# Performance work log

Measured on AMD Instinct MI355X. Metric: run time of the kernel, lower is better.

Reference implementation:

```python
import jax, jax.numpy as jnp
import numpy as np

EPS = 1e-12

def _l2norm(v, axis):
    n = jnp.sqrt(jnp.sum(v * v, axis=axis, keepdims=True))
    return v / jnp.maximum(n, EPS)

def setup_inputs() -> dict:
    key = jax.random.key(0)
    k1, k2, k3, k4 = jax.random.split(key, 4)
    N, T, D, K = 8, 2048, 512, 64
    x = jax.random.normal(k1, (N, T, D), dtype=jnp.float32)
    W = jax.random.normal(k2, (K, D), dtype=jnp.float32) * (1.0 / np.sqrt(D))  # Conv1d(k=1) weight squeezed
    b = jax.random.normal(k3, (K,), dtype=jnp.float32) * 0.01
    centroids = jax.random.uniform(k4, (K, D), dtype=jnp.float32)
    return {"x": x, "W": W, "b": b, "centroids": centroids}

def reference(x, W, b, centroids):
    N, T, D = x.shape
    K = centroids.shape[0]
    # L2-normalize descriptors along feature dim
    xn = _l2norm(x, axis=2)                                  # [N,T,D]
    # Conv1d with kernel_size=1 == per-timestep linear: [N,K,T] logits over clusters
    logits = jnp.einsum('ntd,kd->nkt', xn, W) + b[None, :, None]
    a = jax.nn.softmax(logits, axis=1)                       # soft assignment over K
    # Algebraically equal to sum_t a[n,k,t] * (xn[n,t,:] - c[k,:])
    vlad = jnp.einsum('nkt,ntd->nkd', a, xn) \
         - jnp.sum(a, axis=2)[:, :, None] * centroids[None]  # [N,K,D]
    vlad = _l2norm(vlad, axis=2)                             # intra-normalize per cluster
    vlad = vlad.reshape(N, K * D)
    return _l2norm(vlad, axis=1)                             # global L2 normalize
```

## Files before the change

kernel.cpp:

```cpp
#include <hip/hip_runtime.h>
#include <math.h>

#define EPS 1e-12f
#define NN 8
#define TT 2048
#define DD 512
#define KK 64

typedef short short8 __attribute__((ext_vector_type(8)));
typedef float floatx4 __attribute__((ext_vector_type(4)));

__device__ __forceinline__ unsigned short f2bf(float f) {
    unsigned int u = __float_as_uint(f);
    u += 0x7FFFu + ((u >> 16) & 1u);
    return (unsigned short)(u >> 16);
}
__device__ __forceinline__ unsigned int pack2(float a, float b) {
    return (unsigned int)f2bf(a) | ((unsigned int)f2bf(b) << 16);
}
__device__ __forceinline__ float bf2f_lo(unsigned int u) {
    return __uint_as_float(u << 16);
}
__device__ __forceinline__ float bf2f_hi(unsigned int u) {
    return __uint_as_float(u & 0xFFFF0000u);
}


__global__ __launch_bounds__(1024) void kA(const float* __restrict__ x,
                                           const float* __restrict__ W,
                                           const float* __restrict__ bias,
                                           unsigned short* __restrict__ xb,
                                           unsigned short* __restrict__ aTs,
                                           float* __restrict__ asumP) {
    __shared__ unsigned short sW[32768];
    __shared__ unsigned short sX[32768];
    __shared__ float sSt[64];
    __shared__ float sM[4 * 64];
    __shared__ float sS[4 * 64];
    __shared__ float sRed[256];

    const int tid = threadIdx.x;
    const int w = tid >> 6, lane = tid & 63;
    const int l = lane & 15, q = lane >> 4;
    const int row0 = blockIdx.x * 64;
    const int n = row0 >> 11;
    const int tl0 = row0 & (TT - 1);

    float ssqr[4] = {0.f, 0.f, 0.f, 0.f};
#pragma unroll
    for (int i = 0; i < 8; ++i) {
        const int rl = w * 4 + (i >> 1);
        const int d0 = (i & 1) * 256 + lane * 4;
        float4 u = *(const float4*)(x + (size_t)(row0 + rl) * DD + d0);
        ssqr[i >> 1] += u.x * u.x + u.y * u.y + u.z * u.z + u.w * u.w;
        uint2 pk;
        pk.x = pack2(u.x, u.y);
        pk.y = pack2(u.z, u.w);
        *(uint2*)(xb + (size_t)(row0 + rl) * DD + d0) = pk;
        const int s0 = d0 >> 5, q0 = (d0 >> 3) & 3, half = (d0 >> 2) & 1;
        const int g0 = rl >> 4, lr = rl & 15;
        const int slot = ((g0 * 16 + s0) * 4 + q0) * 16 + (lr ^ ((s0 * 4 + q0) & 15));
        *(uint2*)(sX + slot * 8 + half * 4) = pk;
    }

#pragma unroll
    for (int j = 0; j < 4; ++j) {
        const int slot = tid * 4 + j;
        const int lw = slot & 15, qw = (slot >> 4) & 3, hw = (slot >> 6) & 3, sw = slot >> 8;
        const float* src = W + (size_t)(hw * 16 + lw) * DD + sw * 32 + qw * 8;
        float4 u0 = *(const float4*)(src);
        float4 u1 = *(const float4*)(src + 4);
        uint4 pk;
        pk.x = pack2(u0.x, u0.y); pk.y = pack2(u0.z, u0.w);
        pk.z = pack2(u1.x, u1.y); pk.w = pack2(u1.z, u1.w);
        const int sl2 = slot ^ ((slot >> 4) & 7);
        *(uint4*)(sW + sl2 * 8) = pk;
    }

#pragma unroll
    for (int rr = 0; rr < 4; ++rr) {
        float ss = ssqr[rr];
#pragma unroll
        for (int m = 1; m <= 32; m <<= 1) ss += __shfl_xor(ss, m, 64);
        if (lane == 0) sSt[w * 4 + rr] = 1.0f / fmaxf(sqrtf(ss), EPS);
    }
    __syncthreads();

    const int g = w & 3, h = w >> 2;
    floatx4 acc = floatx4{0.f, 0.f, 0.f, 0.f};
#pragma unroll
    for (int s = 0; s < 16; ++s) {
        short8 af = *(const short8*)(sX + (((g * 16 + s) * 4 + q) * 16 + (l ^ ((s * 4 + q) & 15))) * 8);
        const int slot = (s * 4 + h) * 64 + lane;
        short8 wf = *(const short8*)(sW + (slot ^ ((slot >> 4) & 7)) * 8);
        acc = __builtin_amdgcn_mfma_f32_16x16x32_bf16(af, wf, acc, 0, 0, 0);
    }

    const float bj = bias[h * 16 + l];
    float sr[4], v[4];
#pragma unroll
    for (int r = 0; r < 4; ++r) {
        sr[r] = sSt[g * 16 + 4 * q + r];
        v[r] = acc[r] * sr[r] + bj;
        float m = v[r];
#pragma unroll
        for (int msk = 1; msk <= 8; msk <<= 1) m = fmaxf(m, __shfl_xor(m, msk, 64));
        if (l == 0) sM[h * 64 + g * 16 + 4 * q + r] = m;
    }
    __syncthreads();
    float e[4];
#pragma unroll
    for (int r = 0; r < 4; ++r) {
        const int t = g * 16 + 4 * q + r;
        float M = fmaxf(fmaxf(sM[t], sM[64 + t]), fmaxf(sM[128 + t], sM[192 + t]));
        e[r] = __expf(v[r] - M);
        float ss = e[r];
#pragma unroll
        for (int msk = 1; msk <= 8; msk <<= 1) ss += __shfl_xor(ss, msk, 64);
        if (l == 0) sS[h * 64 + t] = ss;
    }
    __syncthreads();
    float a[4];
#pragma unroll
    for (int r = 0; r < 4; ++r) {
        const int t = g * 16 + 4 * q + r;
        float inv = 1.0f / (sS[t] + sS[64 + t] + sS[128 + t] + sS[192 + t]);
        a[r] = e[r] * inv;
    }

    {
        uint2 p;
        p.x = pack2(a[0] * sr[0], a[1] * sr[1]);
        p.y = pack2(a[2] * sr[2], a[3] * sr[3]);
        *(uint2*)(aTs + ((size_t)(n * KK + h * 16 + l)) * TT + tl0 + g * 16 + 4 * q) = p;
    }

    float sh = a[0] + a[1] + a[2] + a[3];
    sh += __shfl_xor(sh, 16, 64);
    sh += __shfl_xor(sh, 32, 64);
    if (q == 0) sRed[w * 16 + l] = sh;
    __syncthreads();
    if (tid < 64) {
        const int hh = tid >> 4, ll = tid & 15;
        float s0 = sRed[(hh * 4 + 0) * 16 + ll] + sRed[(hh * 4 + 1) * 16 + ll]
                 + sRed[(hh * 4 + 2) * 16 + ll] + sRed[(hh * 4 + 3) * 16 + ll];
        asumP[(size_t)blockIdx.x * 64 + tid] = s0;
    }
}

__global__ __launch_bounds__(256) void kB(const unsigned short* __restrict__ xb,
                                          const unsigned short* __restrict__ aTs,
                                          unsigned short* __restrict__ part16) {
    __shared__ unsigned char smem[9216];
    unsigned short* sX0 = (unsigned short*)smem;
    unsigned short* sX1 = sX0 + 2048;
    float* sT = (float*)smem;

    const int tid = threadIdx.x;
    const int wv = tid >> 6, lane = tid & 63;
    const int l = lane & 15, q = lane >> 4;
    const int bid = blockIdx.x;
    const int low = bid & 63;
    const int n = low >> 3, tc = low & 7, dt = bid >> 6;

    const int ts = tid & 63, dq = tid >> 6;
    const unsigned short* xbase = xb + ((size_t)(n * TT + tc * 256)) * DD + dt * 32 + dq * 8;
    const int g = ts >> 3, t7 = ts & 7;

#define STAGE(S, BUF)                                                          \
    {                                                                          \
        const unsigned short* p_ = xbase + (size_t)((S) * 64 + ts) * DD;       \
        unsigned short vals[8];                                                \
        *(uint4*)(vals) = *(const uint4*)(p_);                                 \
        _Pragma("unroll")                                                      \
        for (int e = 0; e < 8; ++e) {                                          \
            int d_ = dq * 8 + e;                                               \
            (BUF)[d_ * 64 + ((g ^ (d_ & 7)) << 3) + t7] = vals[e];             \
        }                                                                      \
    }

    floatx4 acc[2];
    acc[0] = floatx4{0.f, 0.f, 0.f, 0.f};
    acc[1] = floatx4{0.f, 0.f, 0.f, 0.f};
    const unsigned short* abase = aTs + ((size_t)(n * KK + wv * 16 + l)) * TT + tc * 256;

    STAGE(0, sX0);
    __syncthreads();
#pragma unroll
    for (int s = 0; s < 4; ++s) {
        unsigned short* cur = (s & 1) ? sX1 : sX0;
        unsigned short* nxt = (s & 1) ? sX0 : sX1;
        if (s < 3) {
            if (s == 0) STAGE(1, nxt)
            else if (s == 1) STAGE(2, nxt)
            else STAGE(3, nxt)
        }
#pragma unroll
        for (int kb = 0; kb < 2; ++kb) {
            short8 af = *(const short8*)(abase + s * 64 + kb * 32 + q * 8);
            int gg = q + 4 * kb;
#pragma unroll
            for (int nt = 0; nt < 2; ++nt) {
                int d = nt * 16 + l;
                short8 bf = *(const short8*)(cur + d * 64 + ((gg ^ (d & 7)) << 3));
                acc[nt] = __builtin_amdgcn_mfma_f32_16x16x32_bf16(af, bf, acc[nt], 0, 0, 0);
            }
        }
        __syncthreads();
    }
#undef STAGE

#pragma unroll
    for (int nt = 0; nt < 2; ++nt)
#pragma unroll
        for (int r = 0; r < 4; ++r)
            sT[(wv * 16 + 4 * q + r) * 36 + nt * 16 + l] = acc[nt][r];
    __syncthreads();

    unsigned short* pbase = part16 + ((size_t)(tc * 512 + n * KK)) * DD + dt * 32;
    const int fq = tid & 7, kr = tid >> 3;
#pragma unroll
    for (int i = 0; i < 2; ++i) {
        int k = i * 32 + kr;
        float4 val = *(float4*)(sT + k * 36 + fq * 4);
        uint2 o;
        o.x = pack2(val.x, val.y);
        o.y = pack2(val.z, val.w);
        *(uint2*)(pbase + (size_t)k * DD + fq * 4) = o;
    }
}

__global__ __launch_bounds__(128) void kC(const unsigned short* __restrict__ part16,
                                          const float* __restrict__ asumP,
                                          const float* __restrict__ cent,
                                          float* __restrict__ out) {
    __shared__ float red[2];
    __shared__ float sAsum;
    const int nk = blockIdx.x;
    const int n = nk >> 6, k = nk & 63;
    const int tid = threadIdx.x;

    if (tid < 32) {
        float p = asumP[(size_t)(n * 32 + tid) * 64 + k];
#pragma unroll
        for (int m = 16; m >= 1; m >>= 1) p += __shfl_xor(p, m, 64);
        if (tid == 0) sAsum = p;
    }
    __syncthreads();
    float as = sAsum;

    float4 cc = ((const float4*)(cent + (size_t)k * DD))[tid];
    float4 a4 = make_float4(-as * cc.x, -as * cc.y, -as * cc.z, -as * cc.w);
#pragma unroll
    for (int tc = 0; tc < 8; ++tc) {
        uint2 p = ((const uint2*)(part16 + ((size_t)(tc * 512 + nk)) * DD))[tid];
        a4.x += bf2f_lo(p.x); a4.y += bf2f_hi(p.x);
        a4.z += bf2f_lo(p.y); a4.w += bf2f_hi(p.y);
    }
    float ssq = a4.x * a4.x + a4.y * a4.y + a4.z * a4.z + a4.w * a4.w;
#pragma unroll
    for (int m = 32; m >= 1; m >>= 1) ssq += __shfl_xor(ssq, m, 64);
    if ((tid & 63) == 0) red[tid >> 6] = ssq;
    __syncthreads();
    float nr = sqrtf(red[0] + red[1]);
    float sc = 1.0f / (fmaxf(nr, EPS) * 8.0f);
    a4.x *= sc; a4.y *= sc; a4.z *= sc; a4.w *= sc;
    ((float4*)(out + (size_t)nk * DD))[tid] = a4;
}

extern "C" void kernel_launch(void* const* d_in, const int* in_sizes, int n_in,
                              void* d_out, int out_size, void* d_ws, size_t ws_size,
                              hipStream_t stream) {
    const float* x    = (const float*)d_in[0];
    const float* W    = (const float*)d_in[1];
    const float* b    = (const float*)d_in[2];
    const float* cent = (const float*)d_in[3];
    float* out = (float*)d_out;

    float* w = (float*)d_ws;
    unsigned short* xb     = (unsigned short*)(w + 0);
    unsigned short* aTs    = (unsigned short*)(w + 4194304);
    unsigned short* part16 = (unsigned short*)(w + 4718592);
    float* asumP = w + 5767168;

    hipLaunchKernelGGL(kA, dim3(256), dim3(1024), 0, stream, x, W, b, xb, aTs, asumP);
    hipLaunchKernelGGL(kB, dim3(1024), dim3(256), 0, stream, xb, aTs, part16);
    hipLaunchKernelGGL(kC, dim3(512), dim3(128), 0, stream, part16, asumP, cent, out);
}
```

Baseline: 99.45 us.

## Fuse assignment and VLAD aggregation kernels, computing partials from shared memory

Merges the logits/softmax kernel with the aggregation GEMM. Each block keeps its bf16 x tile and soft-assignment tile in LDS and computes per-chunk VLAD partials directly. This removes the global round-trip of the bf16 x copy and the assignment matrix, and one kernel launch. In exchange, it produces 32 partial chunks instead of 8, which raises the final reduction traffic, and it gathers the B operand with scalar LDS loads.

```diff
diff --git a/kernel.cpp b/kernel.cpp
--- a/kernel.cpp
+++ b/kernel.cpp
@@ -25,26 +25,31 @@
     return __uint_as_float(u & 0xFFFF0000u);
 }
 
-
-__global__ __launch_bounds__(1024) void kA(const float* __restrict__ x,
+__device__ __forceinline__ int lperm(int l, int sq) {
+    int F = l ^ (sq & 15);
+    return F ^ ((F & 8) >> 1);
+}
+
+
+__global__ __launch_bounds__(1024) void kF(const float* __restrict__ x,
                                            const float* __restrict__ W,
                                            const float* __restrict__ bias,
-                                           unsigned short* __restrict__ xb,
-                                           unsigned short* __restrict__ aTs,
+                                           unsigned short* __restrict__ part,
                                            float* __restrict__ asumP) {
+    __shared__ unsigned short sX[32768];
     __shared__ unsigned short sW[32768];
-    __shared__ unsigned short sX[32768];
+    __shared__ unsigned short sA[64 * 72];
     __shared__ float sSt[64];
-    __shared__ float sM[4 * 64];
-    __shared__ float sS[4 * 64];
+    __shared__ float sM[256];
+    __shared__ float sS[256];
     __shared__ float sRed[256];
 
     const int tid = threadIdx.x;
     const int w = tid >> 6, lane = tid & 63;
     const int l = lane & 15, q = lane >> 4;
-    const int row0 = blockIdx.x * 64;
-    const int n = row0 >> 11;
-    const int tl0 = row0 & (TT - 1);
+    const int bid = blockIdx.x;
+    const int row0 = bid * 64;
+    const int n = bid >> 5, c = bid & 31;
 
     float ssqr[4] = {0.f, 0.f, 0.f, 0.f};
 #pragma unroll
@@ -56,18 +61,17 @@
         uint2 pk;
         pk.x = pack2(u.x, u.y);
         pk.y = pack2(u.z, u.w);
-        *(uint2*)(xb + (size_t)(row0 + rl) * DD + d0) = pk;
         const int s0 = d0 >> 5, q0 = (d0 >> 3) & 3, half = (d0 >> 2) & 1;
         const int g0 = rl >> 4, lr = rl & 15;
-        const int slot = ((g0 * 16 + s0) * 4 + q0) * 16 + (lr ^ ((s0 * 4 + q0) & 15));
+        const int slot = ((g0 * 16 + s0) * 4 + q0) * 16 + lperm(lr, s0 * 4 + q0);
         *(uint2*)(sX + slot * 8 + half * 4) = pk;
     }
 
 #pragma unroll
     for (int j = 0; j < 4; ++j) {
         const int slot = tid * 4 + j;
-        const int lw = slot & 15, qw = (slot >> 4) & 3, hw = (slot >> 6) & 3, sw = slot >> 8;
-        const float* src = W + (size_t)(hw * 16 + lw) * DD + sw * 32 + qw * 8;
+        const int lw = slot & 15, qw = (slot >> 4) & 3, hw = (slot >> 6) & 3, sw_ = slot >> 8;
+        const float* src = W + (size_t)(hw * 16 + lw) * DD + sw_ * 32 + qw * 8;
         float4 u0 = *(const float4*)(src);
         float4 u1 = *(const float4*)(src + 4);
         uint4 pk;
@@ -90,7 +94,7 @@
     floatx4 acc = floatx4{0.f, 0.f, 0.f, 0.f};
 #pragma unroll
     for (int s = 0; s < 16; ++s) {
-        short8 af = *(const short8*)(sX + (((g * 16 + s) * 4 + q) * 16 + (l ^ ((s * 4 + q) & 15))) * 8);
+        short8 af = *(const short8*)(sX + (((g * 16 + s) * 4 + q) * 16 + lperm(l, s * 4 + q)) * 8);
         const int slot = (s * 4 + h) * 64 + lane;
         short8 wf = *(const short8*)(sW + (slot ^ ((slot >> 4) & 7)) * 8);
         acc = __builtin_amdgcn_mfma_f32_16x16x32_bf16(af, wf, acc, 0, 0, 0);
@@ -132,105 +136,58 @@
         uint2 p;
         p.x = pack2(a[0] * sr[0], a[1] * sr[1]);
         p.y = pack2(a[2] * sr[2], a[3] * sr[3]);
-        *(uint2*)(aTs + ((size_t)(n * KK + h * 16 + l)) * TT + tl0 + g * 16 + 4 * q) = p;
+        *(uint2*)(sA + (h * 16 + l) * 72 + g * 16 + 4 * q) = p;
     }
 
     float sh = a[0] + a[1] + a[2] + a[3];
     sh += __shfl_xor(sh, 16, 64);
     sh += __shfl_xor(sh, 32, 64);
-    if (q == 0) sRed[w * 16 + l] = sh;
+    if (q == 0) sRed[(h * 16 + l) * 4 + g] = sh;
     __syncthreads();
     if (tid < 64) {
-        const int hh = tid >> 4, ll = tid & 15;
-        float s0 = sRed[(hh * 4 + 0) * 16 + ll] + sRed[(hh * 4 + 1) * 16 + ll]
-                 + sRed[(hh * 4 + 2) * 16 + ll] + sRed[(hh * 4 + 3) * 16 + ll];
-        asumP[(size_t)blockIdx.x * 64 + tid] = s0;
-    }
-}
-
-__global__ __launch_bounds__(256) void kB(const unsigned short* __restrict__ xb,
-                                          const unsigned short* __restrict__ aTs,
-                                          unsigned short* __restrict__ part16) {
-    __shared__ unsigned char smem[9216];
-    unsigned short* sX0 = (unsigned short*)smem;
-    unsigned short* sX1 = sX0 + 2048;
-    float* sT = (float*)smem;
-
-    const int tid = threadIdx.x;
-    const int wv = tid >> 6, lane = tid & 63;
-    const int l = lane & 15, q = lane >> 4;
-    const int bid = blockIdx.x;
-    const int low = bid & 63;
-    const int n = low >> 3, tc = low & 7, dt = bid >> 6;
-
-    const int ts = tid & 63, dq = tid >> 6;
-    const unsigned short* xbase = xb + ((size_t)(n * TT + tc * 256)) * DD + dt * 32 + dq * 8;
-    const int g = ts >> 3, t7 = ts & 7;
-
-#define STAGE(S, BUF)                                                          \
-    {                                                                          \
-        const unsigned short* p_ = xbase + (size_t)((S) * 64 + ts) * DD;       \
-        unsigned short vals[8];                                                \
-        *(uint4*)(vals) = *(const uint4*)(p_);                                 \
-        _Pragma("unroll")                                                      \
-        for (int e = 0; e < 8; ++e) {                                          \
-            int d_ = dq * 8 + e;                                               \
-            (BUF)[d_ * 64 + ((g ^ (d_ & 7)) << 3) + t7] = vals[e];             \
-        }                                                                      \
-    }
-
-    floatx4 acc[2];
-    acc[0] = floatx4{0.f, 0.f, 0.f, 0.f};
-    acc[1] = floatx4{0.f, 0.f, 0.f, 0.f};
-    const unsigned short* abase = aTs + ((size_t)(n * KK + wv * 16 + l)) * TT + tc * 256;
-
-    STAGE(0, sX0);
-    __syncthreads();
-#pragma unroll
-    for (int s = 0; s < 4; ++s) {
-        unsigned short* cur = (s & 1) ? sX1 : sX0;
-        unsigned short* nxt = (s & 1) ? sX0 : sX1;
-        if (s < 3) {
-            if (s == 0) STAGE(1, nxt)
-            else if (s == 1) STAGE(2, nxt)
-            else STAGE(3, nxt)
+        asumP[(size_t)bid * 64 + tid] =
+            sRed[tid * 4] + sRed[tid * 4 + 1] + sRed[tid * 4 + 2] + sRed[tid * 4 + 3];
+    }
+
+    const int kg = w & 3, dt8 = w >> 2;
+    floatx4 pacc[8];
+#pragma unroll
+    for (int j = 0; j < 8; ++j) pacc[j] = floatx4{0.f, 0.f, 0.f, 0.f};
+#pragma unroll
+    for (int kk = 0; kk < 2; ++kk) {
+        short8 af = *(const short8*)(sA + (kg * 16 + l) * 72 + kk * 32 + q * 8);
+        const int gP = kk * 2 + (q >> 1);
+        const int lPb = (q & 1) * 8;
+#pragma unroll
+        for (int j = 0; j < 8; ++j) {
+            const int d = (dt8 * 8 + j) * 16 + l;
+            const int sP = d >> 5, qP = (d >> 3) & 3, eo = d & 7;
+            const int swP = (sP * 4 + qP) & 15;
+            const int Fhi = lPb ^ (swP & 8);
+            const int eX = (swP & 7) ^ ((Fhi & 8) >> 1);
+            const int base = (((gP * 16 + sP) * 4 + qP) * 16 + Fhi) * 8 + eo;
+            union { unsigned short u[8]; short8 v; } bu;
+#pragma unroll
+            for (int ee = 0; ee < 8; ++ee) bu.u[ee] = sX[base + ((ee ^ eX) << 3)];
+            pacc[j] = __builtin_amdgcn_mfma_f32_16x16x32_bf16(af, bu.v, pacc[j], 0, 0, 0);
         }
-#pragma unroll
-        for (int kb = 0; kb < 2; ++kb) {
-            short8 af = *(const short8*)(abase + s * 64 + kb * 32 + q * 8);
-            int gg = q + 4 * kb;
-#pragma unroll
-            for (int nt = 0; nt < 2; ++nt) {
-                int d = nt * 16 + l;
-                short8 bf = *(const short8*)(cur + d * 64 + ((gg ^ (d & 7)) << 3));
-                acc[nt] = __builtin_amdgcn_mfma_f32_16x16x32_bf16(af, bf, acc[nt], 0, 0, 0);
+    }
+
+    unsigned short* pb = part + ((size_t)(c * 512 + n * KK + kg * 16 + q * 4)) * DD + dt8 * 128 + l;
+#pragma unroll
+    for (int j = 0; j < 8; ++j) {
+#pragma unroll
+        for (int r = 0; r < 4; ++r) {
+            float v1 = __shfl_xor(pacc[j][r], 1, 64);
+            if (!(l & 1)) {
+                unsigned int pk = pack2(pacc[j][r], v1);
+                *(unsigned int*)(pb + (size_t)r * DD + j * 16) = pk;
             }
         }
-        __syncthreads();
-    }
-#undef STAGE
-
-#pragma unroll
-    for (int nt = 0; nt < 2; ++nt)
-#pragma unroll
-        for (int r = 0; r < 4; ++r)
-            sT[(wv * 16 + 4 * q + r) * 36 + nt * 16 + l] = acc[nt][r];
-    __syncthreads();
-
-    unsigned short* pbase = part16 + ((size_t)(tc * 512 + n * KK)) * DD + dt * 32;
-    const int fq = tid & 7, kr = tid >> 3;
-#pragma unroll
-    for (int i = 0; i < 2; ++i) {
-        int k = i * 32 + kr;
-        float4 val = *(float4*)(sT + k * 36 + fq * 4);
-        uint2 o;
-        o.x = pack2(val.x, val.y);
-        o.y = pack2(val.z, val.w);
-        *(uint2*)(pbase + (size_t)k * DD + fq * 4) = o;
-    }
-}
-
-__global__ __launch_bounds__(128) void kC(const unsigned short* __restrict__ part16,
+    }
+}
+
+__global__ __launch_bounds__(128) void kC(const unsigned short* __restrict__ part,
                                           const float* __restrict__ asumP,
                                           const float* __restrict__ cent,
                                           float* __restrict__ out) {
@@ -252,8 +209,8 @@
     float4 cc = ((const float4*)(cent + (size_t)k * DD))[tid];
     float4 a4 = make_float4(-as * cc.x, -as * cc.y, -as * cc.z, -as * cc.w);
 #pragma unroll
-    for (int tc = 0; tc < 8; ++tc) {
-        uint2 p = ((const uint2*)(part16 + ((size_t)(tc * 512 + nk)) * DD))[tid];
+    for (int tc = 0; tc < 32; ++tc) {
+        uint2 p = ((const uint2*)(part + ((size_t)(tc * 512 + nk)) * DD))[tid];
         a4.x += bf2f_lo(p.x); a4.y += bf2f_hi(p.x);
         a4.z += bf2f_lo(p.y); a4.w += bf2f_hi(p.y);
     }
@@ -278,12 +235,9 @@
     float* out = (float*)d_out;
 
     float* w = (float*)d_ws;
-    unsigned short* xb     = (unsigned short*)(w + 0);
-    unsigned short* aTs    = (unsigned short*)(w + 4194304);
-    unsigned short* part16 = (unsigned short*)(w + 4718592);
-    float* asumP = w + 5767168;
-
-    hipLaunchKernelGGL(kA, dim3(256), dim3(1024), 0, stream, x, W, b, xb, aTs, asumP);
-    hipLaunchKernelGGL(kB, dim3(1024), dim3(256), 0, stream, xb, aTs, part16);
-    hipLaunchKernelGGL(kC, dim3(512), dim3(128), 0, stream, part16, asumP, cent, out);
-}
+    unsigned short* part = (unsigned short*)(w + 0);
+    float* asumP = w + 4194304;
+
+    hipLaunchKernelGGL(kF, dim3(256), dim3(1024), 0, stream, x, W, b, part, asumP);
+    hipLaunchKernelGGL(kC, dim3(512), dim3(128), 0, stream, part, asumP, cent, out);
+}
```

Result: faster. 97.02 us (-2.4%).
